# Kernel tuning notes

Measured on AMD Instinct MI355X. Metric: run time of the kernel, lower is better.

Reference implementation:

```python
import jax, jax.numpy as jnp
import numpy as np

N_NODES = 50000

def _gat_layer(x, src, dst, W, a_l, a_r, bias, alpha, agg, act, n_nodes):
    # x: [N, in]; W: [in, H*F]; a_l, a_r: [H, F]; bias: [H*F]
    H, F = a_l.shape
    z = (x @ W).reshape(n_nodes, H, F)                      # [N,H,F]
    el = jnp.einsum('nhf,hf->nh', z, a_l)                   # [N,H]
    er = jnp.einsum('nhf,hf->nh', z, a_r)                   # [N,H]
    e = jax.nn.leaky_relu(el[src] + er[dst], alpha)         # [E,H]
    # segment softmax over in-edges of each destination node
    m = jax.ops.segment_max(e, dst, num_segments=n_nodes)   # [N,H]
    ex = jnp.exp(e - m[dst])                                # [E,H]
    s = jax.ops.segment_sum(ex, dst, num_segments=n_nodes)  # [N,H]
    attn = ex / jnp.maximum(s[dst], 1e-9)                   # [E,H]
    msg = attn[:, :, None] * z[src]                         # [E,H,F]
    h = jax.ops.segment_sum(msg, dst, num_segments=n_nodes) # [N,H,F]
    # identity residual (in_feats == H*F) as in DGL GATConv
    h = h + x.reshape(n_nodes, -1, F)
    h = h + bias.reshape(1, H, F)
    if agg == 'flatten':
        h = h.reshape(n_nodes, H * F)
    else:  # mean over heads
        h = h.mean(axis=1)
    if act is not None:
        h = act(h)
    return h


def setup_inputs() -> dict:
    key = jax.random.key(0)
    ks = jax.random.split(key, 14)
    N, E, D = N_NODES, 800000, 128
    H, F = 4, 32
    sc_in = 1.0 / np.sqrt(D)
    sc_h = 1.0 / np.sqrt(H * F)
    inp = {
        'feats': jax.random.normal(ks[0], (N, D), jnp.float32),
        'src': jax.random.randint(ks[1], (E,), 0, N),
        'dst': jax.random.randint(ks[2], (E,), 0, N),
        'W1': jax.random.normal(ks[3], (D, H * F), jnp.float32) * sc_in,
        'al1': jax.random.normal(ks[4], (H, F), jnp.float32) * sc_h,
        'ar1': jax.random.normal(ks[5], (H, F), jnp.float32) * sc_h,
        'b1': jnp.zeros((H * F,), jnp.float32),
        'W2': jax.random.normal(ks[6], (H * F, H * F), jnp.float32) * sc_h,
        'al2': jax.random.normal(ks[7], (H, F), jnp.float32) * sc_h,
        'ar2': jax.random.normal(ks[8], (H, F), jnp.float32) * sc_h,
        'b2': jnp.zeros((H * F,), jnp.float32),
        'Wp': jax.random.normal(ks[9], (F, 1), jnp.float32) / np.sqrt(F),
        'bp': jnp.zeros((1,), jnp.float32),
    }
    return inp


def reference(feats, src, dst, W1, al1, ar1, b1, W2, al2, ar2, b2, Wp, bp):
    h = _gat_layer(feats, src, dst, W1, al1, ar1, b1, 0.2, 'flatten', jax.nn.elu, N_NODES)
    h = _gat_layer(h, src, dst, W2, al2, ar2, b2, 0.2, 'mean', None, N_NODES)
    return h @ Wp + bp  # [N, 1]
```

## Files before the change

kernel.cpp:

```cpp
#include <hip/hip_runtime.h>
#include <hip/hip_bf16.h>

#define NN 50000
#define NE 800000
#define HF 128

#define OFF_FLAG   0u
#define OFF_ROWPTR 256u
#define OFF_BSUM   200272u
#define OFF_BOFF   200480u
#define OFF_SYNC   200680u
#define OFF_ADJ    601088u
#define OFF_FX     3801088u
#define OFF_WC1    16601088u
#define OFF_WC2    16633856u
#define OFF_PAR    16666624u
#define OFF_Z      16668672u
#define OFF_H1     29468672u
#define OFF_EL     42268672u
#define OFF_ER     43068672u
#define OFF_RANK   50000128u

typedef __hip_bfloat16 bf16;
typedef unsigned short us16;

#define PREP_RANK_B   3125
#define PREP_FEATS_B  6250
#define PREP_SMALL_B  132
#define PREP_GRID     (PREP_RANK_B + PREP_FEATS_B + PREP_SMALL_B)

#define NB_SCAN 49
#define GP_PLACE_B 3125
#define GEMM_B 782

typedef __attribute__((ext_vector_type(8))) short bf16x8;
typedef __attribute__((ext_vector_type(4))) float f32x4;

__device__ __forceinline__ float us2f(us16 u) {
  union { unsigned int i; float f; } c; c.i = ((unsigned int)u) << 16; return c.f;
}
__device__ __forceinline__ us16 f2us(float f) {
  bf16 h = __float2bfloat16(f);
  union { bf16 h; us16 u; } c; c.h = h; return c.u;
}
__device__ __forceinline__ float blo(unsigned v) {
  union { unsigned i; float f; } c; c.i = v << 16; return c.f;
}
__device__ __forceinline__ float bhi(unsigned v) {
  union { unsigned i; float f; } c; c.i = v & 0xffff0000u; return c.f;
}
__device__ __forceinline__ unsigned pk2(float a, float b) {
  return (unsigned)f2us(a) | ((unsigned)f2us(b) << 16);
}

__device__ __forceinline__ int detect_f32(const us16* __restrict__ u) {
  int t = threadIdx.x;
  int mx = 0;
  for (int i = t; i < 2048; i += 256) {
    int e = (u[i] >> 7) & 0xFF;
    mx = mx > e ? mx : e;
  }
#pragma unroll
  for (int m = 32; m >= 1; m >>= 1) {
    int o = __shfl_xor(mx, m);
    mx = mx > o ? mx : o;
  }
  __shared__ int sred[4];
  if ((t & 63) == 0) sred[t >> 6] = mx;
  __syncthreads();
  int a = sred[0] > sred[1] ? sred[0] : sred[1];
  int b = sred[2] > sred[3] ? sred[2] : sred[3];
  int r = a > b ? a : b;
  return r >= 135;
}

__global__ __launch_bounds__(256) void k_prep(
    const void* __restrict__ feats, us16* __restrict__ fx,
    const void* s0, const void* s1, const void* s2, const void* s3, const void* s4,
    const void* s5, const void* s6, const void* s7, const void* s8, const void* s9,
    us16* d0, us16* d1, us16* d2, us16* d3, us16* d4,
    us16* d5, us16* d6, us16* d7, us16* d8, us16* d9,
    const int* __restrict__ dst, int* __restrict__ fillp, int* __restrict__ rank,
    int* __restrict__ flag, int* __restrict__ sync) {
  int b = blockIdx.x;
  if (b == 0 && threadIdx.x == 0) { sync[0] = 0; sync[1] = 0; }
  if (b < PREP_RANK_B) {
    int e = b * 256 + threadIdx.x;
    if (e < NE) rank[e] = atomicAdd(&fillp[dst[e] * 16], 1);
    return;
  }
  int f = detect_f32((const us16*)s0);
  if (b == PREP_RANK_B && threadIdx.x == 0) *flag = f;
  if (b < PREP_RANK_B + PREP_FEATS_B) {
    int i = ((b - PREP_RANK_B) * 256 + threadIdx.x) * 4;
    if (f) {
      float4 v = *(const float4*)((const float*)feats + i);
      ushort4 o;
      o.x = f2us(v.x); o.y = f2us(v.y); o.z = f2us(v.z); o.w = f2us(v.w);
      *(ushort4*)(fx + i) = o;
    } else {
      *(ushort4*)(fx + i) = *(const ushort4*)((const us16*)feats + i);
    }
  } else {
    const void* sp[10] = {s0, s1, s2, s3, s4, s5, s6, s7, s8, s9};
    us16* dp[10] = {d0, d1, d2, d3, d4, d5, d6, d7, d8, d9};
    const int cnt[10] = {16384, 16384, 128, 128, 128, 128, 128, 128, 32, 1};
    int gid = (b - PREP_RANK_B - PREP_FEATS_B) * 256 + threadIdx.x;
    int base = 0;
#pragma unroll
    for (int p = 0; p < 10; ++p) {
      int loc = gid - base;
      if (loc >= 0 && loc < cnt[p])
        dp[p][loc] = f ? f2us(((const float*)sp[p])[loc]) : ((const us16*)sp[p])[loc];
      base += cnt[p];
    }
  }
}

__global__ __launch_bounds__(1024) void k_scanall(const int* __restrict__ fillp,
                                                  int* __restrict__ bsum,
                                                  int* __restrict__ boff,
                                                  int* __restrict__ rowptr,
                                                  int* __restrict__ sync) {
  __shared__ int part[1024];
  int t = threadIdx.x, b = blockIdx.x;
  int i = b * 1024 + t;
  int d = (i < NN) ? fillp[i * 16] : 0;
  part[t] = d;
  __syncthreads();
  for (int off = 1; off < 1024; off <<= 1) {
    int v = (t >= off) ? part[t - off] : 0;
    __syncthreads();
    part[t] += v;
    __syncthreads();
  }
  int incl = part[t];
  if (t == 1023) {
    bsum[b] = incl;
    __threadfence();
    atomicAdd(&sync[0], 1);
  }
  if (b == 0) {
    __syncthreads();
    if (t == 0) {
      while (atomicAdd(&sync[0], 0) < NB_SCAN) { }
    }
    __syncthreads();
    if (t < 64) {
      int v = (t < NB_SCAN) ? bsum[t] : 0;
      int orig = v;
#pragma unroll
      for (int off = 1; off < 64; off <<= 1) {
        int u = __shfl_up(v, off);
        if (t >= off) v += u;
      }
      if (t < NB_SCAN) boff[t] = v - orig;
      if (t == 0) rowptr[NN] = NE;
    }
    __syncthreads();
    if (t == 0) {
      __threadfence();
      atomicExch(&sync[1], 1);
    }
  }
  if (t == 0) {
    while (atomicAdd(&sync[1], 0) == 0) { }
  }
  __syncthreads();
  if (i < NN) rowptr[i] = boff[b] + incl - d;
}

__device__ __forceinline__ void gemm_body(const us16* __restrict__ X,
                                          const us16* __restrict__ W,
                                          us16* __restrict__ Z,
                                          const us16* __restrict__ al,
                                          const us16* __restrict__ ar,
                                          float* __restrict__ el,
                                          float* __restrict__ er, int blk) {
  __shared__ us16 Wl[HF * HF];
  int tid = threadIdx.x;
  for (int e = tid; e < HF * HF; e += 256) {
    int k = e >> 7, n = e & 127;
    int d = ((((k >> 5) * 8 + (n >> 4)) * 4 + ((k >> 3) & 3)) * 16 + (n & 15)) * 8 + (k & 7);
    Wl[d] = W[e];
  }
  __syncthreads();

  int w = tid >> 6;
  int lane = tid & 63;
  int q = lane >> 4;
  int c = lane & 15;
  int m0 = blk * 64 + w * 16;

  int rA = m0 + c;
  if (rA >= NN) rA = NN - 1;
  const us16* xrow = X + (size_t)rA * HF;

  f32x4 acc[8] = {};
#pragma unroll
  for (int s = 0; s < 4; ++s) {
    bf16x8 a = *(const bf16x8*)&xrow[s * 32 + q * 8];
#pragma unroll
    for (int t = 0; t < 8; ++t) {
      bf16x8 bb = *(const bf16x8*)&Wl[((((s * 8) + t) * 4 + q) * 16 + c) * 8];
      acc[t] = __builtin_amdgcn_mfma_f32_16x16x32_bf16(a, bb, acc[t], 0, 0, 0);
    }
  }

#pragma unroll
  for (int reg = 0; reg < 4; ++reg) {
    int row = m0 + q * 4 + reg;
    if (row < NN) {
      us16* zrow = Z + (size_t)row * HF;
#pragma unroll
      for (int t = 0; t < 8; ++t) zrow[t * 16 + c] = f2us(acc[t][reg]);
    }
  }

  float alv[8], arv[8];
#pragma unroll
  for (int t = 0; t < 8; ++t) {
    alv[t] = us2f(al[t * 16 + c]);
    arv[t] = us2f(ar[t * 16 + c]);
  }
#pragma unroll
  for (int reg = 0; reg < 4; ++reg) {
    int row = m0 + q * 4 + reg;
    float pl[4], pr[4];
#pragma unroll
    for (int h = 0; h < 4; ++h) {
      pl[h] = acc[2 * h][reg] * alv[2 * h] + acc[2 * h + 1][reg] * alv[2 * h + 1];
      pr[h] = acc[2 * h][reg] * arv[2 * h] + acc[2 * h + 1][reg] * arv[2 * h + 1];
    }
#pragma unroll
    for (int m = 1; m < 16; m <<= 1) {
#pragma unroll
      for (int h = 0; h < 4; ++h) {
        pl[h] += __shfl_xor(pl[h], m);
        pr[h] += __shfl_xor(pr[h], m);
      }
    }
    if (row < NN) {
      int cc = c & 3;
      float vl = cc == 0 ? pl[0] : cc == 1 ? pl[1] : cc == 2 ? pl[2] : pl[3];
      float vr = cc == 0 ? pr[0] : cc == 1 ? pr[1] : cc == 2 ? pr[2] : pr[3];
      if (c < 4) el[row * 4 + cc] = vl;
      else if (c < 8) er[row * 4 + cc] = vr;
    }
  }
}

__global__ __launch_bounds__(256) void k_gemmplace(
    const us16* __restrict__ X, const us16* __restrict__ W, us16* __restrict__ Z,
    const us16* __restrict__ al, const us16* __restrict__ ar,
    float* __restrict__ el, float* __restrict__ er,
    const int* __restrict__ src, const int* __restrict__ dst,
    const int* __restrict__ rowptr, const int* __restrict__ rank,
    int* __restrict__ adj) {
  int b = blockIdx.x;
  if (b < GP_PLACE_B) {
    int e = b * 256 + threadIdx.x;
    if (e < NE) adj[rowptr[dst[e]] + rank[e]] = src[e];
    return;
  }
  gemm_body(X, W, Z, al, ar, el, er, b - GP_PLACE_B);
}

__global__ __launch_bounds__(256) void k_gemm(const us16* __restrict__ X,
                                              const us16* __restrict__ W,
                                              us16* __restrict__ Z,
                                              const us16* __restrict__ al,
                                              const us16* __restrict__ ar,
                                              float* __restrict__ el,
                                              float* __restrict__ er) {
  gemm_body(X, W, Z, al, ar, el, er, blockIdx.x);
}

template <int LAYER>
__global__ __launch_bounds__(256) void k_agg(
    const us16* __restrict__ Z, const float* __restrict__ el,
    const float* __restrict__ er, const int* __restrict__ rowptr,
    const int* __restrict__ adj, const us16* __restrict__ resid,
    const us16* __restrict__ bias, us16* __restrict__ Hout,
    const us16* __restrict__ Wp, const us16* __restrict__ bp,
    void* __restrict__ out, const int* __restrict__ flag) {
  int n = blockIdx.x * 4 + (threadIdx.x >> 6);
  int lane = threadIdx.x & 63;
  int g = lane >> 4;
  int p = lane & 15;
  int hl = p >> 2;
  int f0 = p * 8;
  int begin = rowptr[n];
  int deg = rowptr[n + 1] - begin;
  float erh = er[n * 4 + hl];

  float acc[8] = {};
  float ssum = 0.f;
  int i = g;
  for (; i + 4 < deg; i += 8) {
    int s0 = adj[begin + i];
    int s1 = adj[begin + i + 4];
    float l0 = el[s0 * 4 + hl];
    float l1 = el[s1 * 4 + hl];
    uint4 za = *(const uint4*)&Z[(size_t)s0 * HF + f0];
    uint4 zb = *(const uint4*)&Z[(size_t)s1 * HF + f0];
    float sc0 = l0 + erh; sc0 = sc0 > 0.f ? sc0 : 0.2f * sc0;
    float sc1 = l1 + erh; sc1 = sc1 > 0.f ? sc1 : 0.2f * sc1;
    float ex0 = __expf(sc0);
    float ex1 = __expf(sc1);
    ssum += ex0 + ex1;
    acc[0] = fmaf(ex0, blo(za.x), acc[0]); acc[1] = fmaf(ex0, bhi(za.x), acc[1]);
    acc[2] = fmaf(ex0, blo(za.y), acc[2]); acc[3] = fmaf(ex0, bhi(za.y), acc[3]);
    acc[4] = fmaf(ex0, blo(za.z), acc[4]); acc[5] = fmaf(ex0, bhi(za.z), acc[5]);
    acc[6] = fmaf(ex0, blo(za.w), acc[6]); acc[7] = fmaf(ex0, bhi(za.w), acc[7]);
    acc[0] = fmaf(ex1, blo(zb.x), acc[0]); acc[1] = fmaf(ex1, bhi(zb.x), acc[1]);
    acc[2] = fmaf(ex1, blo(zb.y), acc[2]); acc[3] = fmaf(ex1, bhi(zb.y), acc[3]);
    acc[4] = fmaf(ex1, blo(zb.z), acc[4]); acc[5] = fmaf(ex1, bhi(zb.z), acc[5]);
    acc[6] = fmaf(ex1, blo(zb.w), acc[6]); acc[7] = fmaf(ex1, bhi(zb.w), acc[7]);
  }
  if (i < deg) {
    int s = adj[begin + i];
    float sc = el[s * 4 + hl] + erh;
    sc = sc > 0.f ? sc : 0.2f * sc;
    float ex = __expf(sc);
    ssum += ex;
    uint4 zq = *(const uint4*)&Z[(size_t)s * HF + f0];
    acc[0] = fmaf(ex, blo(zq.x), acc[0]); acc[1] = fmaf(ex, bhi(zq.x), acc[1]);
    acc[2] = fmaf(ex, blo(zq.y), acc[2]); acc[3] = fmaf(ex, bhi(zq.y), acc[3]);
    acc[4] = fmaf(ex, blo(zq.z), acc[4]); acc[5] = fmaf(ex, bhi(zq.z), acc[5]);
    acc[6] = fmaf(ex, blo(zq.w), acc[6]); acc[7] = fmaf(ex, bhi(zq.w), acc[7]);
  }
  ssum += __shfl_xor(ssum, 16); ssum += __shfl_xor(ssum, 32);
#pragma unroll
  for (int j = 0; j < 8; ++j) {
    acc[j] += __shfl_xor(acc[j], 16);
    acc[j] += __shfl_xor(acc[j], 32);
  }
  float inv = 1.f / fmaxf(ssum, 1e-9f);

  uint4 xq = *(const uint4*)&resid[(size_t)n * HF + f0];
  uint4 bq = *(const uint4*)&bias[f0];
  float t0 = fmaf(acc[0], inv, blo(xq.x) + blo(bq.x));
  float t1 = fmaf(acc[1], inv, bhi(xq.x) + bhi(bq.x));
  float t2 = fmaf(acc[2], inv, blo(xq.y) + blo(bq.y));
  float t3 = fmaf(acc[3], inv, bhi(xq.y) + bhi(bq.y));
  float t4 = fmaf(acc[4], inv, blo(xq.z) + blo(bq.z));
  float t5 = fmaf(acc[5], inv, bhi(xq.z) + bhi(bq.z));
  float t6 = fmaf(acc[6], inv, blo(xq.w) + blo(bq.w));
  float t7 = fmaf(acc[7], inv, bhi(xq.w) + bhi(bq.w));

  if (LAYER == 1) {
    t0 = t0 > 0.f ? t0 : __expf(t0) - 1.f;
    t1 = t1 > 0.f ? t1 : __expf(t1) - 1.f;
    t2 = t2 > 0.f ? t2 : __expf(t2) - 1.f;
    t3 = t3 > 0.f ? t3 : __expf(t3) - 1.f;
    t4 = t4 > 0.f ? t4 : __expf(t4) - 1.f;
    t5 = t5 > 0.f ? t5 : __expf(t5) - 1.f;
    t6 = t6 > 0.f ? t6 : __expf(t6) - 1.f;
    t7 = t7 > 0.f ? t7 : __expf(t7) - 1.f;
    if (g == 0) {
      uint4 o;
      o.x = pk2(t0, t1); o.y = pk2(t2, t3); o.z = pk2(t4, t5); o.w = pk2(t6, t7);
      *(uint4*)&Hout[(size_t)n * HF + f0] = o;
    }
  } else {
    t0 += __shfl_xor(t0, 4); t0 += __shfl_xor(t0, 8);
    t1 += __shfl_xor(t1, 4); t1 += __shfl_xor(t1, 8);
    t2 += __shfl_xor(t2, 4); t2 += __shfl_xor(t2, 8);
    t3 += __shfl_xor(t3, 4); t3 += __shfl_xor(t3, 8);
    t4 += __shfl_xor(t4, 4); t4 += __shfl_xor(t4, 8);
    t5 += __shfl_xor(t5, 4); t5 += __shfl_xor(t5, 8);
    t6 += __shfl_xor(t6, 4); t6 += __shfl_xor(t6, 8);
    t7 += __shfl_xor(t7, 4); t7 += __shfl_xor(t7, 8);
    int fw = (p & 3) * 8;
    float pr = 0.25f * (t0 * us2f(Wp[fw]) + t1 * us2f(Wp[fw + 1]) +
                        t2 * us2f(Wp[fw + 2]) + t3 * us2f(Wp[fw + 3]) +
                        t4 * us2f(Wp[fw + 4]) + t5 * us2f(Wp[fw + 5]) +
                        t6 * us2f(Wp[fw + 6]) + t7 * us2f(Wp[fw + 7]));
    pr += __shfl_xor(pr, 1); pr += __shfl_xor(pr, 2);
    if (lane == 0) {
      float res = pr + us2f(bp[0]);
      if (*flag) ((float*)out)[n] = res;
      else ((us16*)out)[n] = f2us(res);
    }
  }
}

extern "C" void kernel_launch(void* const* d_in, const int* in_sizes, int n_in,
                              void* d_out, int out_size, void* d_ws, size_t ws_size,
                              hipStream_t stream) {
  const int* src = (const int*)d_in[1];
  const int* dst = (const int*)d_in[2];
  char* ws = (char*)d_ws;
  int* flag   = (int*)(ws + OFF_FLAG);
  int* rowptr = (int*)(ws + OFF_ROWPTR);
  int* bsum   = (int*)(ws + OFF_BSUM);
  int* boff   = (int*)(ws + OFF_BOFF);
  int* sync   = (int*)(ws + OFF_SYNC);
  int* adj    = (int*)(ws + OFF_ADJ);
  us16* fx    = (us16*)(ws + OFF_FX);
  us16* wc1   = (us16*)(ws + OFF_WC1);
  us16* wc2   = (us16*)(ws + OFF_WC2);
  us16* al1   = (us16*)(ws + OFF_PAR + 0);
  us16* ar1   = (us16*)(ws + OFF_PAR + 256);
  us16* b1    = (us16*)(ws + OFF_PAR + 512);
  us16* al2   = (us16*)(ws + OFF_PAR + 768);
  us16* ar2   = (us16*)(ws + OFF_PAR + 1024);
  us16* b2    = (us16*)(ws + OFF_PAR + 1280);
  us16* wp    = (us16*)(ws + OFF_PAR + 1536);
  us16* bp    = (us16*)(ws + OFF_PAR + 1792);
  us16* z     = (us16*)(ws + OFF_Z);
  us16* h1    = (us16*)(ws + OFF_H1);
  float* el   = (float*)(ws + OFF_EL);
  float* er   = (float*)(ws + OFF_ER);
  int* fillp  = (int*)(ws + OFF_H1);
  int* rank   = (int*)(ws + OFF_RANK);

  hipMemsetAsync(fillp, 0, (size_t)NN * 16 * 4, stream);

  hipLaunchKernelGGL(k_prep, dim3(PREP_GRID), dim3(256), 0, stream,
                     d_in[0], fx,
                     d_in[3], d_in[7], d_in[4], d_in[5], d_in[6],
                     d_in[8], d_in[9], d_in[10], d_in[11], d_in[12],
                     wc1, wc2, al1, ar1, b1, al2, ar2, b2, wp, bp,
                     dst, fillp, rank, flag, sync);

  hipLaunchKernelGGL(k_scanall, dim3(NB_SCAN), dim3(1024), 0, stream,
                     fillp, bsum, boff, rowptr, sync);

  hipLaunchKernelGGL(k_gemmplace, dim3(GP_PLACE_B + GEMM_B), dim3(256), 0, stream,
                     fx, wc1, z, al1, ar1, el, er, src, dst, rowptr, rank, adj);

  hipLaunchKernelGGL((k_agg<1>), dim3(NN / 4), dim3(256), 0, stream, z, el, er, rowptr, adj,
                     fx, b1, h1, (us16*)nullptr, (us16*)nullptr, (void*)nullptr, flag);
  hipLaunchKernelGGL(k_gemm, dim3(GEMM_B), dim3(256), 0, stream, h1, wc2, z,
                     al2, ar2, el, er);
  hipLaunchKernelGGL((k_agg<2>), dim3(NN / 4), dim3(256), 0, stream, z, el, er, rowptr, adj,
                     h1, b2, (us16*)nullptr, wp, bp, d_out, flag);
}
```

Before: 250.7 us.

## Fuse input conversion into GEMM and move edge placement into scan kernel

Removes the separate feats/weight bf16 conversion pass: the layer-1 GEMM now reads fp32 inputs directly and converts them in registers, and it runs inside the prep kernel alongside the degree counting. Edge placement into the CSR adjacency moves into the scan kernel after a grid-wide spin barrier, which drops one kernel launch. The aggregation kernels read the residual, bias and projection weights straight from the original inputs in either precision. This cuts the feats conversion traffic and one launch, but it relies on all 49 scan blocks being resident at once, and placement now runs on only 49 blocks instead of 3125.

```diff
diff --git a/kernel.cpp b/kernel.cpp
--- a/kernel.cpp
+++ b/kernel.cpp
@@ -11,27 +11,20 @@
 #define OFF_BOFF   200480u
 #define OFF_SYNC   200680u
 #define OFF_ADJ    601088u
-#define OFF_FX     3801088u
-#define OFF_WC1    16601088u
-#define OFF_WC2    16633856u
-#define OFF_PAR    16666624u
 #define OFF_Z      16668672u
 #define OFF_H1     29468672u
 #define OFF_EL     42268672u
 #define OFF_ER     43068672u
 #define OFF_RANK   50000128u
+#define OFF_FILLP  54000128u
 
 typedef __hip_bfloat16 bf16;
 typedef unsigned short us16;
 
-#define PREP_RANK_B   3125
-#define PREP_FEATS_B  6250
-#define PREP_SMALL_B  132
-#define PREP_GRID     (PREP_RANK_B + PREP_FEATS_B + PREP_SMALL_B)
-
+#define PREP_RANK_B 3125
+#define PREP_GEMM_B 782
+#define PREP_GRID   (PREP_RANK_B + PREP_GEMM_B)
 #define NB_SCAN 49
-#define GP_PLACE_B 3125
-#define GEMM_B 782
 
 typedef __attribute__((ext_vector_type(8))) short bf16x8;
 typedef __attribute__((ext_vector_type(4))) float f32x4;
@@ -74,54 +67,124 @@
   return r >= 135;
 }
 
+__device__ __forceinline__ void gemm_body(const void* __restrict__ Xv,
+                                          const void* __restrict__ Wv,
+                                          us16* __restrict__ Z,
+                                          const void* __restrict__ alp,
+                                          const void* __restrict__ arp,
+                                          float* __restrict__ el,
+                                          float* __restrict__ er,
+                                          int blk, int fx, int fw) {
+  __shared__ us16 Wl[HF * HF];
+  int tid = threadIdx.x;
+  const us16* Wu = (const us16*)Wv;
+  const float* Wf = (const float*)Wv;
+  for (int e = tid; e < HF * HF; e += 256) {
+    us16 v = fw ? f2us(Wf[e]) : Wu[e];
+    int k = e >> 7, n = e & 127;
+    int d = ((((k >> 5) * 8 + (n >> 4)) * 4 + ((k >> 3) & 3)) * 16 + (n & 15)) * 8 + (k & 7);
+    Wl[d] = v;
+  }
+  __syncthreads();
+
+  int w = tid >> 6;
+  int lane = tid & 63;
+  int q = lane >> 4;
+  int c = lane & 15;
+  int m0 = blk * 64 + w * 16;
+
+  int rA = m0 + c;
+  if (rA >= NN) rA = NN - 1;
+
+  f32x4 acc[8] = {};
+#pragma unroll
+  for (int s = 0; s < 4; ++s) {
+    bf16x8 a;
+    if (fx) {
+      const float* xr = (const float*)Xv + (size_t)rA * HF + s * 32 + q * 8;
+      float4 xa = *(const float4*)xr;
+      float4 xb = *(const float4*)(xr + 4);
+      a[0] = (short)f2us(xa.x); a[1] = (short)f2us(xa.y);
+      a[2] = (short)f2us(xa.z); a[3] = (short)f2us(xa.w);
+      a[4] = (short)f2us(xb.x); a[5] = (short)f2us(xb.y);
+      a[6] = (short)f2us(xb.z); a[7] = (short)f2us(xb.w);
+    } else {
+      a = *(const bf16x8*)((const us16*)Xv + (size_t)rA * HF + s * 32 + q * 8);
+    }
+#pragma unroll
+    for (int t = 0; t < 8; ++t) {
+      bf16x8 bb = *(const bf16x8*)&Wl[((((s * 8) + t) * 4 + q) * 16 + c) * 8];
+      acc[t] = __builtin_amdgcn_mfma_f32_16x16x32_bf16(a, bb, acc[t], 0, 0, 0);
+    }
+  }
+
+#pragma unroll
+  for (int reg = 0; reg < 4; ++reg) {
+    int row = m0 + q * 4 + reg;
+    if (row < NN) {
+      us16* zrow = Z + (size_t)row * HF;
+#pragma unroll
+      for (int t = 0; t < 8; ++t) zrow[t * 16 + c] = f2us(acc[t][reg]);
+    }
+  }
+
+  float alv[8], arv[8];
+#pragma unroll
+  for (int t = 0; t < 8; ++t) {
+    int idx = t * 16 + c;
+    alv[t] = fw ? ((const float*)alp)[idx] : us2f(((const us16*)alp)[idx]);
+    arv[t] = fw ? ((const float*)arp)[idx] : us2f(((const us16*)arp)[idx]);
+  }
+#pragma unroll
+  for (int reg = 0; reg < 4; ++reg) {
+    int row = m0 + q * 4 + reg;
+    float pl[4], pr[4];
+#pragma unroll
+    for (int h = 0; h < 4; ++h) {
+      pl[h] = acc[2 * h][reg] * alv[2 * h] + acc[2 * h + 1][reg] * alv[2 * h + 1];
+      pr[h] = acc[2 * h][reg] * arv[2 * h] + acc[2 * h + 1][reg] * arv[2 * h + 1];
+    }
+#pragma unroll
+    for (int m = 1; m < 16; m <<= 1) {
+#pragma unroll
+      for (int h = 0; h < 4; ++h) {
+        pl[h] += __shfl_xor(pl[h], m);
+        pr[h] += __shfl_xor(pr[h], m);
+      }
+    }
+    if (row < NN) {
+      int cc = c & 3;
+      float vl = cc == 0 ? pl[0] : cc == 1 ? pl[1] : cc == 2 ? pl[2] : pl[3];
+      float vr = cc == 0 ? pr[0] : cc == 1 ? pr[1] : cc == 2 ? pr[2] : pr[3];
+      if (c < 4) el[row * 4 + cc] = vl;
+      else if (c < 8) er[row * 4 + cc] = vr;
+    }
+  }
+}
+
 __global__ __launch_bounds__(256) void k_prep(
-    const void* __restrict__ feats, us16* __restrict__ fx,
-    const void* s0, const void* s1, const void* s2, const void* s3, const void* s4,
-    const void* s5, const void* s6, const void* s7, const void* s8, const void* s9,
-    us16* d0, us16* d1, us16* d2, us16* d3, us16* d4,
-    us16* d5, us16* d6, us16* d7, us16* d8, us16* d9,
+    const void* __restrict__ feats, const void* __restrict__ w1,
+    us16* __restrict__ Z, const void* __restrict__ al1, const void* __restrict__ ar1,
+    float* __restrict__ el, float* __restrict__ er,
     const int* __restrict__ dst, int* __restrict__ fillp, int* __restrict__ rank,
     int* __restrict__ flag, int* __restrict__ sync) {
   int b = blockIdx.x;
-  if (b == 0 && threadIdx.x == 0) { sync[0] = 0; sync[1] = 0; }
+  if (b == 0 && threadIdx.x == 0) { sync[0] = 0; sync[1] = 0; sync[2] = 0; }
   if (b < PREP_RANK_B) {
     int e = b * 256 + threadIdx.x;
     if (e < NE) rank[e] = atomicAdd(&fillp[dst[e] * 16], 1);
     return;
   }
-  int f = detect_f32((const us16*)s0);
+  int f = detect_f32((const us16*)w1);
   if (b == PREP_RANK_B && threadIdx.x == 0) *flag = f;
-  if (b < PREP_RANK_B + PREP_FEATS_B) {
-    int i = ((b - PREP_RANK_B) * 256 + threadIdx.x) * 4;
-    if (f) {
-      float4 v = *(const float4*)((const float*)feats + i);
-      ushort4 o;
-      o.x = f2us(v.x); o.y = f2us(v.y); o.z = f2us(v.z); o.w = f2us(v.w);
-      *(ushort4*)(fx + i) = o;
-    } else {
-      *(ushort4*)(fx + i) = *(const ushort4*)((const us16*)feats + i);
-    }
-  } else {
-    const void* sp[10] = {s0, s1, s2, s3, s4, s5, s6, s7, s8, s9};
-    us16* dp[10] = {d0, d1, d2, d3, d4, d5, d6, d7, d8, d9};
-    const int cnt[10] = {16384, 16384, 128, 128, 128, 128, 128, 128, 32, 1};
-    int gid = (b - PREP_RANK_B - PREP_FEATS_B) * 256 + threadIdx.x;
-    int base = 0;
-#pragma unroll
-    for (int p = 0; p < 10; ++p) {
-      int loc = gid - base;
-      if (loc >= 0 && loc < cnt[p])
-        dp[p][loc] = f ? f2us(((const float*)sp[p])[loc]) : ((const us16*)sp[p])[loc];
-      base += cnt[p];
-    }
-  }
-}
-
-__global__ __launch_bounds__(1024) void k_scanall(const int* __restrict__ fillp,
-                                                  int* __restrict__ bsum,
-                                                  int* __restrict__ boff,
-                                                  int* __restrict__ rowptr,
-                                                  int* __restrict__ sync) {
+  gemm_body(feats, w1, Z, al1, ar1, el, er, b - PREP_RANK_B, f, f);
+}
+
+__global__ __launch_bounds__(1024) void k_scanplace(
+    const int* __restrict__ fillp, int* __restrict__ bsum, int* __restrict__ boff,
+    int* __restrict__ rowptr, int* __restrict__ sync,
+    const int* __restrict__ src, const int* __restrict__ dst,
+    const int* __restrict__ rank, int* __restrict__ adj) {
   __shared__ int part[1024];
   int t = threadIdx.x, b = blockIdx.x;
   int i = b * 1024 + t;
@@ -168,122 +231,38 @@
   }
   __syncthreads();
   if (i < NN) rowptr[i] = boff[b] + incl - d;
-}
-
-__device__ __forceinline__ void gemm_body(const us16* __restrict__ X,
-                                          const us16* __restrict__ W,
-                                          us16* __restrict__ Z,
-                                          const us16* __restrict__ al,
-                                          const us16* __restrict__ ar,
-                                          float* __restrict__ el,
-                                          float* __restrict__ er, int blk) {
-  __shared__ us16 Wl[HF * HF];
-  int tid = threadIdx.x;
-  for (int e = tid; e < HF * HF; e += 256) {
-    int k = e >> 7, n = e & 127;
-    int d = ((((k >> 5) * 8 + (n >> 4)) * 4 + ((k >> 3) & 3)) * 16 + (n & 15)) * 8 + (k & 7);
-    Wl[d] = W[e];
-  }
-  __syncthreads();
-
-  int w = tid >> 6;
-  int lane = tid & 63;
-  int q = lane >> 4;
-  int c = lane & 15;
-  int m0 = blk * 64 + w * 16;
-
-  int rA = m0 + c;
-  if (rA >= NN) rA = NN - 1;
-  const us16* xrow = X + (size_t)rA * HF;
-
-  f32x4 acc[8] = {};
-#pragma unroll
-  for (int s = 0; s < 4; ++s) {
-    bf16x8 a = *(const bf16x8*)&xrow[s * 32 + q * 8];
-#pragma unroll
-    for (int t = 0; t < 8; ++t) {
-      bf16x8 bb = *(const bf16x8*)&Wl[((((s * 8) + t) * 4 + q) * 16 + c) * 8];
-      acc[t] = __builtin_amdgcn_mfma_f32_16x16x32_bf16(a, bb, acc[t], 0, 0, 0);
-    }
-  }
-
-#pragma unroll
-  for (int reg = 0; reg < 4; ++reg) {
-    int row = m0 + q * 4 + reg;
-    if (row < NN) {
-      us16* zrow = Z + (size_t)row * HF;
-#pragma unroll
-      for (int t = 0; t < 8; ++t) zrow[t * 16 + c] = f2us(acc[t][reg]);
-    }
-  }
-
-  float alv[8], arv[8];
-#pragma unroll
-  for (int t = 0; t < 8; ++t) {
-    alv[t] = us2f(al[t * 16 + c]);
-    arv[t] = us2f(ar[t * 16 + c]);
-  }
-#pragma unroll
-  for (int reg = 0; reg < 4; ++reg) {
-    int row = m0 + q * 4 + reg;
-    float pl[4], pr[4];
-#pragma unroll
-    for (int h = 0; h < 4; ++h) {
-      pl[h] = acc[2 * h][reg] * alv[2 * h] + acc[2 * h + 1][reg] * alv[2 * h + 1];
-      pr[h] = acc[2 * h][reg] * arv[2 * h] + acc[2 * h + 1][reg] * arv[2 * h + 1];
-    }
-#pragma unroll
-    for (int m = 1; m < 16; m <<= 1) {
-#pragma unroll
-      for (int h = 0; h < 4; ++h) {
-        pl[h] += __shfl_xor(pl[h], m);
-        pr[h] += __shfl_xor(pr[h], m);
-      }
-    }
-    if (row < NN) {
-      int cc = c & 3;
-      float vl = cc == 0 ? pl[0] : cc == 1 ? pl[1] : cc == 2 ? pl[2] : pl[3];
-      float vr = cc == 0 ? pr[0] : cc == 1 ? pr[1] : cc == 2 ? pr[2] : pr[3];
-      if (c < 4) el[row * 4 + cc] = vl;
-      else if (c < 8) er[row * 4 + cc] = vr;
-    }
-  }
-}
-
-__global__ __launch_bounds__(256) void k_gemmplace(
-    const us16* __restrict__ X, const us16* __restrict__ W, us16* __restrict__ Z,
-    const us16* __restrict__ al, const us16* __restrict__ ar,
-    float* __restrict__ el, float* __restrict__ er,
-    const int* __restrict__ src, const int* __restrict__ dst,
-    const int* __restrict__ rowptr, const int* __restrict__ rank,
-    int* __restrict__ adj) {
-  int b = blockIdx.x;
-  if (b < GP_PLACE_B) {
-    int e = b * 256 + threadIdx.x;
-    if (e < NE) adj[rowptr[dst[e]] + rank[e]] = src[e];
-    return;
-  }
-  gemm_body(X, W, Z, al, ar, el, er, b - GP_PLACE_B);
-}
-
-__global__ __launch_bounds__(256) void k_gemm(const us16* __restrict__ X,
-                                              const us16* __restrict__ W,
-                                              us16* __restrict__ Z,
-                                              const us16* __restrict__ al,
-                                              const us16* __restrict__ ar,
-                                              float* __restrict__ el,
-                                              float* __restrict__ er) {
-  gemm_body(X, W, Z, al, ar, el, er, blockIdx.x);
+  __threadfence();
+  __syncthreads();
+  if (t == 0) {
+    atomicAdd(&sync[2], 1);
+    while (atomicAdd(&sync[2], 0) < NB_SCAN) { }
+  }
+  __syncthreads();
+  const int CHUNK = (NE + NB_SCAN - 1) / NB_SCAN;
+  int e1 = b * CHUNK + CHUNK;
+  if (e1 > NE) e1 = NE;
+  for (int e = b * CHUNK + t; e < e1; e += 1024) {
+    adj[rowptr[dst[e]] + rank[e]] = src[e];
+  }
+}
+
+__global__ __launch_bounds__(256) void k_gemm(
+    const us16* __restrict__ X, const void* __restrict__ W, us16* __restrict__ Z,
+    const void* __restrict__ al, const void* __restrict__ ar,
+    float* __restrict__ el, float* __restrict__ er, const int* __restrict__ flag) {
+  int f = *flag;
+  gemm_body(X, W, Z, al, ar, el, er, blockIdx.x, 0, f);
 }
 
 template <int LAYER>
 __global__ __launch_bounds__(256) void k_agg(
     const us16* __restrict__ Z, const float* __restrict__ el,
     const float* __restrict__ er, const int* __restrict__ rowptr,
-    const int* __restrict__ adj, const us16* __restrict__ resid,
-    const us16* __restrict__ bias, us16* __restrict__ Hout,
-    const us16* __restrict__ Wp, const us16* __restrict__ bp,
+    const int* __restrict__ adj, const void* __restrict__ resid,
+    const void* __restrict__ bias, us16* __restrict__ Hout,
+    const void* __restrict__ Wp, const void* __restrict__ bp,
     void* __restrict__ out, const int* __restrict__ flag) {
+  int f = *flag;
   int n = blockIdx.x * 4 + (threadIdx.x >> 6);
   int lane = threadIdx.x & 63;
   int g = lane >> 4;
@@ -338,16 +317,38 @@
   }
   float inv = 1.f / fmaxf(ssum, 1e-9f);
 
-  uint4 xq = *(const uint4*)&resid[(size_t)n * HF + f0];
-  uint4 bq = *(const uint4*)&bias[f0];
-  float t0 = fmaf(acc[0], inv, blo(xq.x) + blo(bq.x));
-  float t1 = fmaf(acc[1], inv, bhi(xq.x) + bhi(bq.x));
-  float t2 = fmaf(acc[2], inv, blo(xq.y) + blo(bq.y));
-  float t3 = fmaf(acc[3], inv, bhi(xq.y) + bhi(bq.y));
-  float t4 = fmaf(acc[4], inv, blo(xq.z) + blo(bq.z));
-  float t5 = fmaf(acc[5], inv, bhi(xq.z) + bhi(bq.z));
-  float t6 = fmaf(acc[6], inv, blo(xq.w) + blo(bq.w));
-  float t7 = fmaf(acc[7], inv, bhi(xq.w) + bhi(bq.w));
+  float x0, x1, x2, x3, x4, x5, x6, x7;
+  if (LAYER == 1 && f) {
+    const float* xr = (const float*)resid + (size_t)n * HF + f0;
+    float4 a = *(const float4*)xr;
+    float4 b4 = *(const float4*)(xr + 4);
+    x0 = a.x; x1 = a.y; x2 = a.z; x3 = a.w;
+    x4 = b4.x; x5 = b4.y; x6 = b4.z; x7 = b4.w;
+  } else {
+    uint4 xq = *(const uint4*)((const us16*)resid + (size_t)n * HF + f0);
+    x0 = blo(xq.x); x1 = bhi(xq.x); x2 = blo(xq.y); x3 = bhi(xq.y);
+    x4 = blo(xq.z); x5 = bhi(xq.z); x6 = blo(xq.w); x7 = bhi(xq.w);
+  }
+  float bb0, bb1, bb2, bb3, bb4, bb5, bb6, bb7;
+  if (f) {
+    const float* br = (const float*)bias + f0;
+    float4 a = *(const float4*)br;
+    float4 b4 = *(const float4*)(br + 4);
+    bb0 = a.x; bb1 = a.y; bb2 = a.z; bb3 = a.w;
+    bb4 = b4.x; bb5 = b4.y; bb6 = b4.z; bb7 = b4.w;
+  } else {
+    uint4 bq = *(const uint4*)((const us16*)bias + f0);
+    bb0 = blo(bq.x); bb1 = bhi(bq.x); bb2 = blo(bq.y); bb3 = bhi(bq.y);
+    bb4 = blo(bq.z); bb5 = bhi(bq.z); bb6 = blo(bq.w); bb7 = bhi(bq.w);
+  }
+  float t0 = fmaf(acc[0], inv, x0 + bb0);
+  float t1 = fmaf(acc[1], inv, x1 + bb1);
+  float t2 = fmaf(acc[2], inv, x2 + bb2);
+  float t3 = fmaf(acc[3], inv, x3 + bb3);
+  float t4 = fmaf(acc[4], inv, x4 + bb4);
+  float t5 = fmaf(acc[5], inv, x5 + bb5);
+  float t6 = fmaf(acc[6], inv, x6 + bb6);
+  float t7 = fmaf(acc[7], inv, x7 + bb7);
 
   if (LAYER == 1) {
     t0 = t0 > 0.f ? t0 : __expf(t0) - 1.f;
@@ -373,14 +374,24 @@
     t6 += __shfl_xor(t6, 4); t6 += __shfl_xor(t6, 8);
     t7 += __shfl_xor(t7, 4); t7 += __shfl_xor(t7, 8);
     int fw = (p & 3) * 8;
-    float pr = 0.25f * (t0 * us2f(Wp[fw]) + t1 * us2f(Wp[fw + 1]) +
-                        t2 * us2f(Wp[fw + 2]) + t3 * us2f(Wp[fw + 3]) +
-                        t4 * us2f(Wp[fw + 4]) + t5 * us2f(Wp[fw + 5]) +
-                        t6 * us2f(Wp[fw + 6]) + t7 * us2f(Wp[fw + 7]));
+    float w0, w1, w2, w3, w4, w5, w6, w7, bpv;
+    if (f) {
+      const float* wpr = (const float*)Wp + fw;
+      w0 = wpr[0]; w1 = wpr[1]; w2 = wpr[2]; w3 = wpr[3];
+      w4 = wpr[4]; w5 = wpr[5]; w6 = wpr[6]; w7 = wpr[7];
+      bpv = ((const float*)bp)[0];
+    } else {
+      const us16* wpr = (const us16*)Wp + fw;
+      w0 = us2f(wpr[0]); w1 = us2f(wpr[1]); w2 = us2f(wpr[2]); w3 = us2f(wpr[3]);
+      w4 = us2f(wpr[4]); w5 = us2f(wpr[5]); w6 = us2f(wpr[6]); w7 = us2f(wpr[7]);
+      bpv = us2f(((const us16*)bp)[0]);
+    }
+    float pr = 0.25f * (t0 * w0 + t1 * w1 + t2 * w2 + t3 * w3 +
+                        t4 * w4 + t5 * w5 + t6 * w6 + t7 * w7);
     pr += __shfl_xor(pr, 1); pr += __shfl_xor(pr, 2);
     if (lane == 0) {
-      float res = pr + us2f(bp[0]);
-      if (*flag) ((float*)out)[n] = res;
+      float res = pr + bpv;
+      if (f) ((float*)out)[n] = res;
       else ((us16*)out)[n] = f2us(res);
     }
   }
@@ -398,43 +409,27 @@
   int* boff   = (int*)(ws + OFF_BOFF);
   int* sync   = (int*)(ws + OFF_SYNC);
   int* adj    = (int*)(ws + OFF_ADJ);
-  us16* fx    = (us16*)(ws + OFF_FX);
-  us16* wc1   = (us16*)(ws + OFF_WC1);
-  us16* wc2   = (us16*)(ws + OFF_WC2);
-  us16* al1   = (us16*)(ws + OFF_PAR + 0);
-  us16* ar1   = (us16*)(ws + OFF_PAR + 256);
-  us16* b1    = (us16*)(ws + OFF_PAR + 512);
-  us16* al2   = (us16*)(ws + OFF_PAR + 768);
-  us16* ar2   = (us16*)(ws + OFF_PAR + 1024);
-  us16* b2    = (us16*)(ws + OFF_PAR + 1280);
-  us16* wp    = (us16*)(ws + OFF_PAR + 1536);
-  us16* bp    = (us16*)(ws + OFF_PAR + 1792);
   us16* z     = (us16*)(ws + OFF_Z);
   us16* h1    = (us16*)(ws + OFF_H1);
   float* el   = (float*)(ws + OFF_EL);
   float* er   = (float*)(ws + OFF_ER);
-  int* fillp  = (int*)(ws + OFF_H1);
   int* rank   = (int*)(ws + OFF_RANK);
+  int* fillp  = (int*)(ws + OFF_FILLP);
 
   hipMemsetAsync(fillp, 0, (size_t)NN * 16 * 4, stream);
 
   hipLaunchKernelGGL(k_prep, dim3(PREP_GRID), dim3(256), 0, stream,
-                     d_in[0], fx,
-                     d_in[3], d_in[7], d_in[4], d_in[5], d_in[6],
-                     d_in[8], d_in[9], d_in[10], d_in[11], d_in[12],
-                     wc1, wc2, al1, ar1, b1, al2, ar2, b2, wp, bp,
+                     d_in[0], d_in[3], z, d_in[4], d_in[5], el, er,
                      dst, fillp, rank, flag, sync);
 
-  hipLaunchKernelGGL(k_scanall, dim3(NB_SCAN), dim3(1024), 0, stream,
-                     fillp, bsum, boff, rowptr, sync);
-
-  hipLaunchKernelGGL(k_gemmplace, dim3(GP_PLACE_B + GEMM_B), dim3(256), 0, stream,
-                     fx, wc1, z, al1, ar1, el, er, src, dst, rowptr, rank, adj);
+  hipLaunchKernelGGL(k_scanplace, dim3(NB_SCAN), dim3(1024), 0, stream,
+                     fillp, bsum, boff, rowptr, sync, src, dst, rank, adj);
 
   hipLaunchKernelGGL((k_agg<1>), dim3(NN / 4), dim3(256), 0, stream, z, el, er, rowptr, adj,
-                     fx, b1, h1, (us16*)nullptr, (us16*)nullptr, (void*)nullptr, flag);
-  hipLaunchKernelGGL(k_gemm, dim3(GEMM_B), dim3(256), 0, stream, h1, wc2, z,
-                     al2, ar2, el, er);
+                     d_in[0], d_in[6], h1, (const void*)nullptr, (const void*)nullptr,
+                     (void*)nullptr, flag);
+  hipLaunchKernelGGL(k_gemm, dim3(PREP_GEMM_B), dim3(256), 0, stream, h1, d_in[7], z,
+                     d_in[8], d_in[9], el, er, flag);
   hipLaunchKernelGGL((k_agg<2>), dim3(NN / 4), dim3(256), 0, stream, z, el, er, rowptr, adj,
-                     h1, b2, (us16*)nullptr, wp, bp, d_out, flag);
-}
+                     h1, d_in[10], (us16*)nullptr, d_in[11], d_in[12], d_out, flag);
+}
```

Result: slower. 319.4 us (+27.4%).
